# Kernel tuning notes

Measured on AMD Instinct MI355X. Metric: run time of the kernel, lower is better.

## Reference

```python
import jax, jax.numpy as jnp
import numpy as np
from jax import lax

BEAM = 4
MAXLEN = 12
V, E, H = 32000, 256, 512
S, B = 512, 8


def lstm_cell(x, h, c, Wih, Whh, bih, bhh):
    # torch gate order: input, forget, cell, output
    g = x @ Wih.T + h @ Whh.T + bih + bhh
    i, f, gg, o = jnp.split(g, 4, axis=-1)
    c2 = jax.nn.sigmoid(f) * c + jax.nn.sigmoid(i) * jnp.tanh(gg)
    return jax.nn.sigmoid(o) * jnp.tanh(c2), c2


def lstm_layer(xs, Wih, Whh, bih, bhh):
    Bn, Hn = xs.shape[1], Whh.shape[1]
    h0 = jnp.zeros((Bn, Hn), xs.dtype)

    def step(carry, x):
        h, c = carry
        h, c = lstm_cell(x, h, c, Wih, Whh, bih, bhh)
        return (h, c), h

    (hT, cT), hs = lax.scan(step, (h0, h0), xs)
    return hs, hT, cT


def setup_inputs():
    key = jax.random.key(0)
    ks = jax.random.split(key, 32)

    def p(i, shape, s=0.08):
        return jax.random.normal(ks[i], shape, jnp.float32) * s

    return {
        'text': jax.random.randint(ks[0], (S, B), 0, V),
        'emb_enc': p(1, (V, E)),
        'emb_dec': p(2, (V, E)),
        'enc_Wih0': p(3, (4 * H, E)), 'enc_Whh0': p(4, (4 * H, H)),
        'enc_bih0': p(5, (4 * H,)), 'enc_bhh0': p(6, (4 * H,)),
        'enc_Wih1': p(7, (4 * H, H)), 'enc_Whh1': p(8, (4 * H, H)),
        'enc_bih1': p(9, (4 * H,)), 'enc_bhh1': p(10, (4 * H,)),
        'dec_Wih': p(11, (4 * H, E)), 'dec_Whh': p(12, (4 * H, H)),
        'dec_bih': p(13, (4 * H,)), 'dec_bhh': p(14, (4 * H,)),
        'Wq': p(15, (H, H)), 'bq': p(16, (H,)),
        'Wk': p(17, (H, H)), 'bk': p(18, (H,)),
        'Wv': p(19, (H, H)), 'bv': p(20, (H,)),
        'Wo': p(21, (H, H)), 'bo': p(22, (H,)),
        'Wout': p(23, (V, H)), 'bout': p(24, (V,)),
    }


def reference(text, emb_enc, emb_dec, enc_Wih0, enc_Whh0, enc_bih0, enc_bhh0,
              enc_Wih1, enc_Whh1, enc_bih1, enc_bhh1,
              dec_Wih, dec_Whh, dec_bih, dec_bhh,
              Wq, bq, Wk, bk, Wv, bv, Wo, bo, Wout, bout):
    # ---- encoder: 2-layer LSTM over source ----
    emb = emb_enc[text]                                   # [S, B, E]
    hs0, h0, c0 = lstm_layer(emb, enc_Wih0, enc_Whh0, enc_bih0, enc_bhh0)
    hs1, h1, c1 = lstm_layer(hs0, enc_Wih1, enc_Whh1, enc_bih1, enc_bhh1)
    enc_hidden = jnp.stack([h0, h1])                      # [L, B, H] final hidden per layer
    k_enc = enc_hidden @ Wk.T + bk                        # precompute encoder K/V projections
    v_enc = enc_hidden @ Wv.T + bv
    scale = 1.0 / jnp.sqrt(jnp.float32(H))

    # ---- beam state: all beams start from last encoder layer state ----
    dec_h = jnp.tile(h1[None], (BEAM, 1, 1))              # [BEAM, B, H]
    dec_c = jnp.tile(c1[None], (BEAM, 1, 1))
    T = MAXLEN + 1
    result = jnp.full((BEAM, T, B), 1, dtype=jnp.int32)   # SOS token = 1
    logits_hist = jnp.zeros((BEAM, T, B, V), jnp.float32).at[:, 0, :, 1].set(1.0)

    def step(carry, t):
        dh, dc, res, lh = carry
        tok = lax.dynamic_slice(res, (0, t, 0), (BEAM, 1, B))[:, 0, :]      # last token [BEAM, B]
        x = emb_dec[tok]                                                    # [BEAM, B, E]
        nh, nc = lstm_cell(x, dh, dc, dec_Wih, dec_Whh, dec_bih, dec_bhh)   # batched over beams
        # single-head attention: query = dec hidden, keys/values = [enc layers ; dec hidden]
        q = nh @ Wq.T + bq
        kd = nh @ Wk.T + bk
        vd = nh @ Wv.T + bv
        keys = jnp.concatenate([jnp.broadcast_to(k_enc[None], (BEAM,) + k_enc.shape), kd[:, None]], axis=1)  # [BEAM, L+1, B, H]
        vals = jnp.concatenate([jnp.broadcast_to(v_enc[None], (BEAM,) + v_enc.shape), vd[:, None]], axis=1)
        scores = jnp.einsum('nbh,nlbh->nbl', q, keys) * scale
        w = jax.nn.softmax(scores, axis=-1)
        ctx = jnp.einsum('nbl,nlbh->nbh', w, vals)
        dec_out = (ctx @ Wo.T + bo) @ Wout.T + bout                          # [BEAM, B, V]
        # per-beam top-k over vocab, then top-k over the BEAM*BEAM candidates
        pv, pt = lax.top_k(dec_out, BEAM)                                    # [BEAM, B, K]
        cand_v = jnp.transpose(pv, (1, 0, 2)).reshape(B, BEAM * BEAM)        # beam-major blocks
        cand_t = jnp.transpose(pt, (1, 0, 2)).reshape(B, BEAM * BEAM)
        _, ti = lax.top_k(cand_v, BEAM)                                      # [B, K]
        old_beam = (ti // BEAM).T                                            # [BEAM, B]
        new_tok = jnp.take_along_axis(cand_t, ti, axis=1).T                  # [BEAM, B]
        # vectorized beam reorder (gather) of state + history
        nh = jnp.take_along_axis(nh, old_beam[:, :, None], axis=0)
        nc = jnp.take_along_axis(nc, old_beam[:, :, None], axis=0)
        res = jnp.take_along_axis(res, old_beam[:, None, :], axis=0)
        lh = jnp.take_along_axis(lh, old_beam[:, None, :, None], axis=0)
        step_log = jnp.take_along_axis(dec_out, old_beam[:, :, None], axis=0)
        res = lax.dynamic_update_slice(res, new_tok[:, None, :].astype(jnp.int32), (0, t + 1, 0))
        lh = lax.dynamic_update_slice(lh, step_log[:, None], (0, t + 1, 0, 0))
        return (nh, nc, res, lh), None

    (dec_h, dec_c, result, logits_hist), _ = lax.scan(
        step, (dec_h, dec_c, result, logits_hist), jnp.arange(MAXLEN))
    output_res = result[0].T                               # [B, T]
    output_logits = jnp.transpose(logits_hist[0], (1, 2, 0))  # [B, V, T]
    return output_res, output_logits
```

## Files before the change

### kernel.cpp

```cpp
#include <hip/hip_runtime.h>
#include <hip/hip_bf16.h>
#include <float.h>


using ull = unsigned long long;

#define SCOPE_AGENT __HIP_MEMORY_SCOPE_AGENT

__device__ __forceinline__ float cLoad(const float* p) {
  return __hip_atomic_load(p, __ATOMIC_RELAXED, SCOPE_AGENT);
}
__device__ __forceinline__ void cStore(float* p, float v) {
  __hip_atomic_store(p, v, __ATOMIC_RELAXED, SCOPE_AGENT);
}
__device__ __forceinline__ int cLoadI(const int* p) {
  return __hip_atomic_load(p, __ATOMIC_RELAXED, SCOPE_AGENT);
}
__device__ __forceinline__ void cStoreI(int* p, int v) {
  __hip_atomic_store(p, v, __ATOMIC_RELAXED, SCOPE_AGENT);
}
__device__ __forceinline__ ull cLoad64(const ull* p) {
  return __hip_atomic_load(p, __ATOMIC_RELAXED, SCOPE_AGENT);
}
__device__ __forceinline__ void cStore64(ull* p, ull v) {
  __hip_atomic_store(p, v, __ATOMIC_RELAXED, SCOPE_AGENT);
}

__device__ __forceinline__ float2 u2f2(ull u) {
  union { ull u; float2 f; } c; c.u = u; return c.f;
}

__device__ __forceinline__ void fbar1(int* fl, int phase) {
  __syncthreads();
  if (threadIdx.x < 32)
    cStoreI(fl + (blockIdx.x * 32 + threadIdx.x) * 32, phase);
  {
    const int* f = fl + (threadIdx.x * 32 + (blockIdx.x >> 3)) * 32;
    while (cLoadI(f) < phase) {}
  }
  __syncthreads();
}

__device__ __forceinline__ float sig_(float x) { return 1.0f / (1.0f + expf(-x)); }

__device__ __forceinline__ void ins4(float* v, int* id, float nv, int ni) {
  if (nv > v[3] || (nv == v[3] && ni < id[3])) {
    v[3] = nv; id[3] = ni;
#pragma unroll
    for (int p = 3; p > 0; --p) {
      bool sw = (v[p] > v[p - 1]) || (v[p] == v[p - 1] && id[p] < id[p - 1]);
      if (sw) {
        float t0 = v[p]; v[p] = v[p - 1]; v[p - 1] = t0;
        int t1 = id[p]; id[p] = id[p - 1]; id[p - 1] = t1;
      }
    }
  }
}

struct EncP {
  const int* text; const float* emb;
  const float* Wih0; const float* Whh0; const float* bih0; const float* bhh0;
  const float* Wih1; const float* Whh1; const float* bih1; const float* bhh1;
  float* h0buf; float* h1buf; int* regF;
  float* h0f; float* h1f; float* c1f;
};

template <int KX>
__device__ void enc_run(const EncP& P, float* xcat, int w, int tid) {
  constexpr int KTOT = KX + 512;
  constexpr int ST = KTOT + 4;
  constexpr int KSL = KTOT / 8;
  constexpr int Q = KSL / 4;
  constexpr int L = (KX == 512) ? 1 : 0;
  __shared__ float part[16 * 8 * 8];
  __shared__ float gl[128];

  const int c0 = (w & 127) * 4;
  const int kh = tid >> 5, col = (tid >> 3) & 3, b = tid & 7;
  const int kbase = kh * KSL;
  const int rep = w >> 3;

  const float* Wih = L ? P.Wih1 : P.Wih0;
  const float* Whh = L ? P.Whh1 : P.Whh0;
  const float4* wih4[4]; const float4* whh4[4];
#pragma unroll
  for (int g = 0; g < 4; ++g) {
    const int row = g * 512 + c0 + col;
    wih4[g] = (const float4*)(Wih + (size_t)row * KX);
    whh4[g] = (const float4*)(Whh + (size_t)row * 512);
  }
  float bsum = 0.f;
  if (tid < 128) {
    const int r = tid >> 3;
    const int row = (r & 3) * 512 + c0 + (r >> 2);
    bsum = (L ? P.bih1[row] + P.bhh1[row] : P.bih0[row] + P.bhh0[row]);
  }
  float creg = 0.f;
  float* myH = L ? P.h1buf : P.h0buf;

  int qx = (KX - kbase) / 4;
  qx = qx < 0 ? 0 : (qx > Q ? Q : qx);

  for (int e = tid; e < 4096; e += 256)
    xcat[(e >> 9) * ST + KX + (e & 511)] = 0.f;
  __syncthreads();

  for (int i = 0; i <= 512; ++i) {
    const bool act = L ? (i >= 1) : (i < 512);
    if (act) {
      const int t = L ? (i - 1) : i;
      float a0 = 0.f, a1 = 0.f, a2 = 0.f, a3 = 0.f;

      if constexpr (KX == 256) {
        for (int e = tid; e < 1024; e += 256) {
          const int b2 = e >> 7, k2 = e & 127;
          const int tokv = P.text[t * 8 + b2];
          *(float2*)(xcat + b2 * ST + 2 * k2) =
              *(const float2*)(P.emb + (size_t)tokv * 256 + 2 * k2);
        }
        __syncthreads();
        const float4* xq = (const float4*)(xcat + b * ST + kbase);
        const int iw = kbase >> 2;
#pragma unroll 4
        for (int q = 0; q < qx; ++q) {
          float4 x = xq[q];
          float4 w0 = wih4[0][iw + q], w1 = wih4[1][iw + q];
          float4 w2 = wih4[2][iw + q], w3 = wih4[3][iw + q];
          a0 = fmaf(w0.x, x.x, a0); a0 = fmaf(w0.y, x.y, a0);
          a0 = fmaf(w0.z, x.z, a0); a0 = fmaf(w0.w, x.w, a0);
          a1 = fmaf(w1.x, x.x, a1); a1 = fmaf(w1.y, x.y, a1);
          a1 = fmaf(w1.z, x.z, a1); a1 = fmaf(w1.w, x.w, a1);
          a2 = fmaf(w2.x, x.x, a2); a2 = fmaf(w2.y, x.y, a2);
          a2 = fmaf(w2.z, x.z, a2); a2 = fmaf(w2.w, x.w, a2);
          a3 = fmaf(w3.x, x.x, a3); a3 = fmaf(w3.y, x.y, a3);
          a3 = fmaf(w3.z, x.z, a3); a3 = fmaf(w3.w, x.w, a3);
        }
      }

      if (i >= 1) {
        const int s = tid;
        if ((s < 128) || (i >= 2)) {
          const int* f = P.regF + (s * 32 + rep) * 32;
          while (cLoadI(f) < i) __builtin_amdgcn_s_sleep(2);
        }
      }
      __syncthreads();

      if constexpr (KX == 512) {
        const ull* x0 = (const ull*)(P.h0buf + ((i + 1) & 1) * 4096);
        for (int e = tid; e < 2048; e += 256) {
          const int b2 = e >> 8, k2 = e & 255;
          *(ull*)(xcat + b2 * ST + 2 * k2) = cLoad64(x0 + b2 * 256 + k2);
        }
        if (i >= 2) {
          const ull* hq = (const ull*)(P.h1buf + (i & 1) * 4096);
          for (int e = tid; e < 2048; e += 256) {
            const int b2 = e >> 8, k2 = e & 255;
            *(ull*)(xcat + b2 * ST + KX + 2 * k2) = cLoad64(hq + b2 * 256 + k2);
          }
        }
      } else {
        if (i >= 1) {
          const ull* hq = (const ull*)(P.h0buf + ((i + 1) & 1) * 4096);
          for (int e = tid; e < 2048; e += 256) {
            const int b2 = e >> 8, k2 = e & 255;
            *(ull*)(xcat + b2 * ST + KX + 2 * k2) = cLoad64(hq + b2 * 256 + k2);
          }
        }
      }
      __syncthreads();

      {
        const float4* xq = (const float4*)(xcat + b * ST + kbase);
        const int iw = kbase >> 2, ih = (kbase - KX) >> 2;
        if constexpr (KX == 512) {
#pragma unroll 4
          for (int q = 0; q < qx; ++q) {
            float4 x = xq[q];
            float4 w0 = wih4[0][iw + q], w1 = wih4[1][iw + q];
            float4 w2 = wih4[2][iw + q], w3 = wih4[3][iw + q];
            a0 = fmaf(w0.x, x.x, a0); a0 = fmaf(w0.y, x.y, a0);
            a0 = fmaf(w0.z, x.z, a0); a0 = fmaf(w0.w, x.w, a0);
            a1 = fmaf(w1.x, x.x, a1); a1 = fmaf(w1.y, x.y, a1);
            a1 = fmaf(w1.z, x.z, a1); a1 = fmaf(w1.w, x.w, a1);
            a2 = fmaf(w2.x, x.x, a2); a2 = fmaf(w2.y, x.y, a2);
            a2 = fmaf(w2.z, x.z, a2); a2 = fmaf(w2.w, x.w, a2);
            a3 = fmaf(w3.x, x.x, a3); a3 = fmaf(w3.y, x.y, a3);
            a3 = fmaf(w3.z, x.z, a3); a3 = fmaf(w3.w, x.w, a3);
          }
        }
#pragma unroll 4
        for (int q = qx; q < Q; ++q) {
          float4 x = xq[q];
          float4 w0 = whh4[0][ih + q], w1 = whh4[1][ih + q];
          float4 w2 = whh4[2][ih + q], w3 = whh4[3][ih + q];
          a0 = fmaf(w0.x, x.x, a0); a0 = fmaf(w0.y, x.y, a0);
          a0 = fmaf(w0.z, x.z, a0); a0 = fmaf(w0.w, x.w, a0);
          a1 = fmaf(w1.x, x.x, a1); a1 = fmaf(w1.y, x.y, a1);
          a1 = fmaf(w1.z, x.z, a1); a1 = fmaf(w1.w, x.w, a1);
          a2 = fmaf(w2.x, x.x, a2); a2 = fmaf(w2.y, x.y, a2);
          a2 = fmaf(w2.z, x.z, a2); a2 = fmaf(w2.w, x.w, a2);
          a3 = fmaf(w3.x, x.x, a3); a3 = fmaf(w3.y, x.y, a3);
          a3 = fmaf(w3.z, x.z, a3); a3 = fmaf(w3.w, x.w, a3);
        }
      }
      part[((col * 4 + 0) * 8 + b) * 8 + kh] = a0;
      part[((col * 4 + 1) * 8 + b) * 8 + kh] = a1;
      part[((col * 4 + 2) * 8 + b) * 8 + kh] = a2;
      part[((col * 4 + 3) * 8 + b) * 8 + kh] = a3;
      __syncthreads();
      if (tid < 128) {
        const int r = tid >> 3, b2 = tid & 7;
        const float4* pp = (const float4*)(part + (r * 8 + b2) * 8);
        float4 p0 = pp[0], p1 = pp[1];
        gl[r * 8 + b2] =
            bsum + (((p0.x + p0.y) + (p0.z + p0.w)) + ((p1.x + p1.y) + (p1.z + p1.w)));
      }
      __syncthreads();
      if (tid < 32) {
        const int cc = tid >> 3, b2 = tid & 7;
        float gi = gl[(cc * 4 + 0) * 8 + b2], gf_ = gl[(cc * 4 + 1) * 8 + b2];
        float gg = gl[(cc * 4 + 2) * 8 + b2], go = gl[(cc * 4 + 3) * 8 + b2];
        float c2 = sig_(gf_) * creg + sig_(gi) * tanhf(gg);
        float hv = sig_(go) * tanhf(c2);
        creg = c2;
        cStore(myH + (t & 1) * 4096 + b2 * 512 + c0 + cc, hv);
        if (t == 511) {
          (L ? P.h1f : P.h0f)[b2 * 512 + c0 + cc] = hv;
          if (L) P.c1f[b2 * 512 + c0 + cc] = c2;
        }
      }
      __syncthreads();
      if (tid < 32) cStoreI(P.regF + (w * 32 + tid) * 32, i + 1);
    }
  }
}

__global__ __launch_bounds__(256, 1) void enc_kernel(EncP P) {
  __shared__ float xcat0[8 * 772];
  __shared__ float xcat1[8 * 1028];
  if (blockIdx.x >> 7) enc_run<512>(P, xcat1, blockIdx.x, threadIdx.x);
  else enc_run<256>(P, xcat0, blockIdx.x, threadIdx.x);
}

__global__ __launch_bounds__(256) void prep_kernel(
    const float* Wk, const float* bk, const float* Wv, const float* bv,
    const float* h0f, const float* h1f, const float* c1f,
    float* kenc, float* venc, float* nhb, float* ncb) {
  const int w = blockIdx.x, tid = threadIdx.x;
  if (w < 64) {
    const int o = w * 256 + tid;
    const int kv = o >> 13, l = (o >> 12) & 1, b = (o >> 9) & 7, c = o & 511;
    const float4* h4 = (const float4*)((l ? h1f : h0f) + b * 512);
    const float4* w4 = (const float4*)((kv ? Wv : Wk) + (size_t)c * 512);
    float s0 = 0.f, s1 = 0.f, s2 = 0.f, s3 = 0.f;
#pragma unroll 8
    for (int k = 0; k < 128; ++k) {
      float4 a = w4[k], x = h4[k];
      s0 = fmaf(a.x, x.x, s0); s1 = fmaf(a.y, x.y, s1);
      s2 = fmaf(a.z, x.z, s2); s3 = fmaf(a.w, x.w, s3);
    }
    (kv ? venc : kenc)[l * 4096 + b * 512 + c] =
        (kv ? bv : bk)[c] + ((s0 + s1) + (s2 + s3));
  } else {
    const int o = (w - 64) * 256 + tid;
    nhb[16384 + o] = h1f[o & 4095];
    ncb[16384 + o] = c1f[o & 4095];
  }
}

__global__ __launch_bounds__(256) void prep2_kernel(
    const float* Wq, const float* Wk, const float* Wv, const float* Wo,
    const float* bq, const float* bk, const float* bv,
    const float* kenc, const float* venc,
    float* At, float* W2, float* u, float* pvec, float* veWo, float* bvo,
    float* sl0, float* sbb) {
  const int w = blockIdx.x, tid = threadIdx.x;
#pragma unroll 1
  for (int sub = 0; sub < 2; ++sub) {
    const int d = 2 * w + sub;
    for (int cc = 0; cc < 2; ++cc) {
      const int c = tid + cc * 256;
      float s0 = 0.f, s1 = 0.f, s2 = 0.f, s3 = 0.f;
      for (int i = 0; i < 512; i += 4) {
        s0 = fmaf(Wk[(i + 0) * 512 + d], Wq[(i + 0) * 512 + c], s0);
        s1 = fmaf(Wk[(i + 1) * 512 + d], Wq[(i + 1) * 512 + c], s1);
        s2 = fmaf(Wk[(i + 2) * 512 + d], Wq[(i + 2) * 512 + c], s2);
        s3 = fmaf(Wk[(i + 3) * 512 + d], Wq[(i + 3) * 512 + c], s3);
      }
      At[(size_t)d * 512 + c] = (s0 + s1) + (s2 + s3);
    }
    for (int cc = 0; cc < 2; ++cc) {
      const int dc = tid + cc * 256;
      float s0 = 0.f, s1 = 0.f, s2 = 0.f, s3 = 0.f;
      const float* wor = Wo + (size_t)d * 512;
      for (int c2 = 0; c2 < 512; c2 += 4) {
        s0 = fmaf(wor[c2 + 0], Wv[(size_t)(c2 + 0) * 512 + dc], s0);
        s1 = fmaf(wor[c2 + 1], Wv[(size_t)(c2 + 1) * 512 + dc], s1);
        s2 = fmaf(wor[c2 + 2], Wv[(size_t)(c2 + 2) * 512 + dc], s2);
        s3 = fmaf(wor[c2 + 3], Wv[(size_t)(c2 + 3) * 512 + dc], s3);
      }
      W2[(size_t)d * 512 + dc] = (s0 + s1) + (s2 + s3);
    }
  }
  if (w == 0) {
    for (int cc = 0; cc < 2; ++cc) {
      const int c = tid + cc * 256;
      float a = 0.f;
      for (int i = 0; i < 512; ++i)
        a += Wq[i * 512 + c] * bk[i] + Wk[i * 512 + c] * bq[i];
      u[c] = a;
    }
  } else if (w <= 32) {
    const int idx = (w - 1) * 256 + tid;
    const int l = idx >> 12, b = (idx >> 9) & 7, c = idx & 511;
    const float* ke = kenc + l * 4096 + b * 512;
    float a = 0.f;
    for (int i = 0; i < 512; ++i) a = fmaf(Wq[i * 512 + c], ke[i], a);
    pvec[idx] = a;
  } else if (w <= 64) {
    const int idx = (w - 33) * 256 + tid;
    const int l = idx >> 12, b = (idx >> 9) & 7, j = idx & 511;
    const float* ve = venc + l * 4096 + b * 512;
    const float* wo = Wo + (size_t)j * 512;
    float a = 0.f;
    for (int c = 0; c < 512; ++c) a = fmaf(wo[c], ve[c], a);
    veWo[idx] = a;
  } else if (w == 65) {
    for (int cc = 0; cc < 2; ++cc) {
      const int j = tid + cc * 256;
      const float* wo = Wo + (size_t)j * 512;
      float a = 0.f;
      for (int c = 0; c < 512; ++c) a = fmaf(wo[c], bv[c], a);
      bvo[j] = a;
    }
  } else if (w == 66) {
    if (tid < 16) {
      const int l = tid >> 3, b = tid & 7;
      const float* ke = kenc + l * 4096 + b * 512;
      float a = 0.f;
      for (int i = 0; i < 512; ++i) a = fmaf(bq[i], ke[i], a);
      sl0[tid] = a;
    } else if (tid == 16) {
      float a = 0.f;
      for (int i = 0; i < 512; ++i) a = fmaf(bq[i], bk[i], a);
      sbb[0] = a;
    }
  }
}

__global__ __launch_bounds__(256) void prep3_kernel(
    const float* Wout, const float* bout, const float* bo, const float* veWo,
    float* E0g, float* E1g, float* bcg) {
  __shared__ float sv[16 * 516 + 512];
  __shared__ float stg[8 * 516];
  const int w = blockIdx.x, tid = threadIdx.x;
  for (int e = tid; e < 8704; e += 256) {
    if (e < 8192) sv[(e >> 9) * 516 + (e & 511)] = veWo[e];
    else sv[16 * 516 + (e - 8192)] = bo[e - 8192];
  }
  const int cbase = w * 125;
  for (int tile = 0; tile < 16; ++tile) {
    const int r0 = tile * 8;
    __syncthreads();
    for (int e = tid; e < 1024; e += 256) {
      const int rr = e >> 7, k4 = e & 127;
      int row = r0 + rr; if (row > 124) row = 124;
      *(float4*)&stg[rr * 516 + k4 * 4] =
          *(const float4*)&Wout[(size_t)(cbase + row) * 512 + k4 * 4];
    }
    __syncthreads();
    if (tid < 136) {
      const int rr = tid / 17, sel = tid - rr * 17;
      const int row = r0 + rr;
      if (row < 125) {
        const float4* a4 = (const float4*)&stg[rr * 516];
        const float4* x4 =
            (const float4*)&sv[sel < 16 ? sel * 516 : 16 * 516];
        float s0 = 0.f, s1 = 0.f, s2 = 0.f, s3 = 0.f;
#pragma unroll 8
        for (int k = 0; k < 128; ++k) {
          float4 a = a4[k], x = x4[k];
          s0 = fmaf(a.x, x.x, s0); s1 = fmaf(a.y, x.y, s1);
          s2 = fmaf(a.z, x.z, s2); s3 = fmaf(a.w, x.w, s3);
        }
        const float s = (s0 + s1) + (s2 + s3);
        const int c = cbase + row;
        if (sel < 16) (sel < 8 ? E0g : E1g)[(size_t)(sel & 7) * 32000 + c] = s;
        else bcg[c] = s + bout[c];
      }
    }
  }
}

struct DecP {
  const float* emb;
  const float* Wih; const float* Whh; const float* bih; const float* bhh;
  const float* Wout;
  const float* At; const float* W2; const float* u; const float* bvo;
  const float* pvec; const float* sl0; const float* sbb;
  const float* E0g; const float* E1g; const float* bcg;
  float* nhb; float* ncb;
  float* vbuf;
  float* part_s;
  ull* pvp;
  int* obh;
  int* res0;
  __hip_bfloat16* hist;
  int* fl;
};

__global__ __launch_bounds__(256, 1) void dec_kernel(DecP P) {
  __shared__ float SM[29600];
  __shared__ float gl[2][4][32];
  __shared__ float slS[32][3];
  __shared__ float wslS[96];
  __shared__ float svv[32][8][4];
  __shared__ int sii[32][8][4];
  __shared__ float rvS[32][4];
  __shared__ int rtS[32][4];
  __shared__ int resS[4][13][8];
  __shared__ int oblS[32];
  __shared__ int tokS[32];
  __shared__ float pscS[32][8];
  __shared__ float nhsS[32][8];

  const int w = blockIdx.x, tid = threadIdx.x;
  float* hs = SM;
  float* tileS = SM;
  float* vqS = SM + 16896;
  float* tvE = SM + 21120;
  int* tiE = (int*)(SM + 25344);
  int ph = 0;

  if (tid < 104) {
    for (int n = 0; n < 4; ++n) resS[n][tid >> 3][tid & 7] = 1;
  }

  auto do_select = [&](int tt) {
    {
      const int r = tid >> 3, ch = tid & 7;
      float m4[4] = {-FLT_MAX, -FLT_MAX, -FLT_MAX, -FLT_MAX};
      int mi[4] = {0x7fffffff, 0x7fffffff, 0x7fffffff, 0x7fffffff};
      for (int g = 0; g < 4; ++g) {
        ull pk[32];
#pragma unroll
        for (int z = 0; z < 32; ++z) {
          const int wg = ch * 32 + g * 8 + (z >> 2);
          pk[z] = cLoad64(P.pvp + wg * 128 + r * 4 + (z & 3));
        }
#pragma unroll
        for (int z = 0; z < 32; ++z)
          ins4(m4, mi, __uint_as_float((unsigned)(pk[z] >> 32)),
               (int)(unsigned)(pk[z] & 0xffffffffu));
      }
#pragma unroll
      for (int k = 0; k < 4; ++k) { svv[r][ch][k] = m4[k]; sii[r][ch][k] = mi[k]; }
    }
    __syncthreads();
    if (tid < 32) {
      float m4[4] = {-FLT_MAX, -FLT_MAX, -FLT_MAX, -FLT_MAX};
      int mi[4] = {0x7fffffff, 0x7fffffff, 0x7fffffff, 0x7fffffff};
      for (int g2 = 0; g2 < 8; ++g2)
#pragma unroll
        for (int k = 0; k < 4; ++k) ins4(m4, mi, svv[tid][g2][k], sii[tid][g2][k]);
#pragma unroll
      for (int k = 0; k < 4; ++k) { rvS[tid][k] = m4[k]; rtS[tid][k] = mi[k]; }
    }
    __syncthreads();
    if (tid < 8) {
      const int b2 = tid;
      unsigned used = 0;
      int obl_[4], tkl_[4];
#pragma unroll
      for (int sel = 0; sel < 4; ++sel) {
        float bestv = -FLT_MAX; int bestj = -1;
        for (int j = 0; j < 16; ++j) {
          if (used & (1u << j)) continue;
          float vv = rvS[(j >> 2) * 8 + b2][j & 3];
          if (vv > bestv) { bestv = vv; bestj = j; }
        }
        used |= 1u << bestj;
        const int obn = bestj >> 2;
        obl_[sel] = obn;
        tkl_[sel] = rtS[obn * 8 + b2][bestj & 3];
        oblS[sel * 8 + b2] = obn;
        tokS[sel * 8 + b2] = tkl_[sel];
        if (w == 0) P.obh[tt * 32 + sel * 8 + b2] = obn;
      }
      if (w == 0) {
        int tmp[4][13];
        for (int n2 = 0; n2 < 4; ++n2)
          for (int s2 = 0; s2 < 13; ++s2) tmp[n2][s2] = resS[obl_[n2]][s2][b2];
        for (int n2 = 0; n2 < 4; ++n2)
          for (int s2 = 0; s2 < 13; ++s2) resS[n2][s2][b2] = tmp[n2][s2];
        for (int n2 = 0; n2 < 4; ++n2) resS[n2][tt + 1][b2] = tkl_[n2];
      }
    }
    __syncthreads();
    if (tt == 11 && w == 0 && tid < 104)
      P.res0[tid] = resS[0][tid >> 3][tid & 7];
  };

  for (int t = 0; t < 12; ++t) {
    const int curOff = (t & 1) * 16384, prevOff = ((t + 1) & 1) * 16384;

    if (t == 0) {
      __syncthreads();
      if (tid < 32) { oblS[tid] = tid >> 3; tokS[tid] = 1; }
      __syncthreads();
    } else {
      do_select(t - 1);
    }
    {
      const int col_l = tid >> 7, gate = (tid >> 5) & 3, nb = tid & 31;
      const int col = 2 * w + col_l;
      const int row = gate * 512 + col;
      for (int e = tid; e < 2048; e += 256) {
        const int nb2 = e >> 6, kf = e & 63;
        float4 v = *((const float4*)(P.emb + (size_t)tokS[nb2] * 256) + kf);
        *((float4*)hs + nb2 * 65 + kf) = v;
      }
      __syncthreads();
      float s0 = 0.f, s1 = 0.f, s2 = 0.f, s3 = 0.f;
      {
        const float4* a4 = (const float4*)(P.Wih + (size_t)row * 256);
        const float4* x4 = (const float4*)hs + nb * 65;
#pragma unroll 8
        for (int k = 0; k < 64; ++k) {
          float4 a = a4[k], x = x4[k];
          s0 = fmaf(a.x, x.x, s0); s1 = fmaf(a.y, x.y, s1);
          s2 = fmaf(a.z, x.z, s2); s3 = fmaf(a.w, x.w, s3);
        }
      }
      float acc = P.bih[row] + P.bhh[row];
      const ull* hsrc = (const ull*)(P.nhb + prevOff);
      const float4* w4row = (const float4*)(P.Whh + (size_t)row * 512);
      for (int ck = 0; ck < 2; ++ck) {
        __syncthreads();
        for (int e = tid; e < 4096; e += 256) {
          const int nb2 = e >> 7, k2 = e & 127;
          const int srow = oblS[nb2] * 8 + (nb2 & 7);
          ull v = cLoad64(hsrc + srow * 256 + ck * 128 + k2);
          *(ull*)(hs + nb2 * 260 + 2 * k2) = v;
        }
        __syncthreads();
        const float4* h4 = (const float4*)hs + nb * 65;
        const float4* w4 = w4row + ck * 64;
#pragma unroll 8
        for (int k = 0; k < 64; ++k) {
          float4 a = w4[k], x = h4[k];
          s0 = fmaf(a.x, x.x, s0); s1 = fmaf(a.y, x.y, s1);
          s2 = fmaf(a.z, x.z, s2); s3 = fmaf(a.w, x.w, s3);
        }
      }
      acc += (s0 + s1) + (s2 + s3);
      gl[col_l][gate][nb] = acc;
      __syncthreads();
      if (tid < 64) {
        const int cc = tid >> 5, nb2 = tid & 31;
        const int col2 = 2 * w + cc;
        float gi = gl[cc][0][nb2], gf_ = gl[cc][1][nb2];
        float gg = gl[cc][2][nb2], go = gl[cc][3][nb2];
        const int srow = oblS[nb2] * 8 + (nb2 & 7);
        float cold = cLoad(P.ncb + prevOff + srow * 512 + col2);
        float c2 = sig_(gf_) * cold + sig_(gi) * tanhf(gg);
        float hv = sig_(go) * tanhf(c2);
        cStore(P.nhb + curOff + nb2 * 512 + col2, hv);
        cStore(P.ncb + curOff + nb2 * 512 + col2, c2);
      }
    }
    fbar1(P.fl, ++ph);

    if (w < 128) {
      const int p = w >> 6, cb = w & 63;
      const int col_l = tid >> 5, nb = tid & 31;
      const int col = cb * 8 + col_l;
      const float* W = (p ? P.W2 : P.At) + (size_t)col * 512;
      float acc = (p ? P.bvo : P.u)[col];
      {
        const float4* w4row = (const float4*)W;
        float s0 = 0.f, s1 = 0.f, s2 = 0.f, s3 = 0.f;
        for (int ck = 0; ck < 2; ++ck) {
          __syncthreads();
          const ull* s8 = (const ull*)(P.nhb + curOff);
          for (int e = tid; e < 4096; e += 256) {
            const int nb2 = e >> 7, k2 = e & 127;
            ull v = cLoad64(s8 + nb2 * 256 + ck * 128 + k2);
            *(ull*)(hs + nb2 * 260 + 2 * k2) = v;
          }
          __syncthreads();
          const float4* h4 = (const float4*)hs + nb * 65;
          const float4* w4 = w4row + ck * 64;
#pragma unroll 8
          for (int k = 0; k < 64; ++k) {
            float4 a = w4[k], x = h4[k];
            s0 = fmaf(a.x, x.x, s0); s1 = fmaf(a.y, x.y, s1);
            s2 = fmaf(a.z, x.z, s2); s3 = fmaf(a.w, x.w, s3);
          }
        }
        acc += (s0 + s1) + (s2 + s3);
      }
      if (p) {
        cStore(P.vbuf + nb * 512 + col, acc);
      } else {
        const float nhv = cLoad(P.nhb + curOff + nb * 512 + col);
        pscS[nb][col_l] = nhv * acc;
        nhsS[nb][col_l] = nhv;
        __syncthreads();
        if (tid < 32) {
          const int nb2 = tid, b = nb2 & 7;
          float s2a = 0.f, l0 = 0.f, l1 = 0.f;
#pragma unroll
          for (int i2 = 0; i2 < 8; ++i2) {
            s2a += pscS[nb2][i2];
            const float nv = nhsS[nb2][i2];
            l0 = fmaf(nv, P.pvec[b * 512 + cb * 8 + i2], l0);
            l1 = fmaf(nv, P.pvec[4096 + b * 512 + cb * 8 + i2], l1);
          }
          cStore(P.part_s + (0 * 32 + nb2) * 64 + cb, l0);
          cStore(P.part_s + (1 * 32 + nb2) * 64 + cb, l1);
          cStore(P.part_s + (2 * 32 + nb2) * 64 + cb, s2a);
        }
      }
    }
    fbar1(P.fl, ++ph);

    {
      const int cbase = w * 125;
      if (tid < 96) {
        const int nb = tid / 3, l = tid - (tid / 3) * 3, b = nb & 7;
        const ull* ps = (const ull*)(P.part_s + (l * 32 + nb) * 64);
        ull pk[32];
#pragma unroll
        for (int z = 0; z < 32; ++z) pk[z] = cLoad64(ps + z);
        float s = 0.f;
#pragma unroll
        for (int z = 0; z < 32; ++z) { float2 f = u2f2(pk[z]); s += f.x + f.y; }
        const float bias = (l < 2) ? P.sl0[l * 8 + b] : P.sbb[0];
        slS[nb][l] = (s + bias) * (1.0f / sqrtf(512.0f));
      }
      __syncthreads();
      if (tid < 32) {
        float a = slS[tid][0], b2 = slS[tid][1], c3 = slS[tid][2];
        float m = fmaxf(a, fmaxf(b2, c3));
        float e0 = expf(a - m), e1 = expf(b2 - m), e2 = expf(c3 - m);
        float inv = 1.0f / (e0 + e1 + e2);
        wslS[tid * 3 + 0] = e0 * inv;
        wslS[tid * 3 + 1] = e1 * inv;
        wslS[tid * 3 + 2] = e2 * inv;
      }
      const int rg = tid >> 3, ng = tid & 7;
      float acc[4][4];
#pragma unroll
      for (int i = 0; i < 4; ++i)
#pragma unroll
        for (int j = 0; j < 4; ++j) acc[i][j] = 0.f;
      for (int q = 0; q < 4; ++q) {
        __syncthreads();
        for (int e = tid; e < 1024; e += 256) {
          const int nb = e >> 5, kf = e & 31;
          ull u0 = cLoad64((const ull*)(P.vbuf + nb * 512 + q * 128 + kf * 4));
          ull u1 = cLoad64((const ull*)(P.vbuf + nb * 512 + q * 128 + kf * 4 + 2));
          float2 a = u2f2(u0), b2 = u2f2(u1);
          float4 v = {a.x, a.y, b2.x, b2.y};
          *(float4*)(vqS + (nb & 3) * 1056 + (nb >> 2) * 132 + kf * 4) = v;
        }
        for (int it = 0; it < 16; ++it) {
          const int idx = it * 256 + tid;
          if (idx < 4000) {
            const int r = idx >> 5, kf = idx & 31;
            float4 v = *(const float4*)(P.Wout + (size_t)(cbase + r) * 512 +
                                        q * 128 + kf * 4);
            *(float4*)(tileS + (r & 3) * 4224 + (r >> 2) * 132 + kf * 4) = v;
          }
        }
        __syncthreads();
        for (int kf = 0; kf < 32; ++kf) {
          float4 xv[4], wv[4];
#pragma unroll
          for (int j = 0; j < 4; ++j)
            xv[j] = *(const float4*)(vqS + j * 1056 + ng * 132 + kf * 4);
#pragma unroll
          for (int i = 0; i < 4; ++i)
            wv[i] = *(const float4*)(tileS + i * 4224 + rg * 132 + kf * 4);
#pragma unroll
          for (int i = 0; i < 4; ++i)
#pragma unroll
            for (int j = 0; j < 4; ++j) {
              float a = acc[i][j];
              a = fmaf(wv[i].x, xv[j].x, a); a = fmaf(wv[i].y, xv[j].y, a);
              a = fmaf(wv[i].z, xv[j].z, a); a = fmaf(wv[i].w, xv[j].w, a);
              acc[i][j] = a;
            }
        }
      }
      __syncthreads();
      float w0w[4], w1w[4], w2w[4];
#pragma unroll
      for (int j = 0; j < 4; ++j) {
        const int nb = ng * 4 + j;
        w0w[j] = wslS[nb * 3 + 0]; w1w[j] = wslS[nb * 3 + 1]; w2w[j] = wslS[nb * 3 + 2];
      }
      float v4[4][4]; int i4[4][4];
#pragma unroll
      for (int j = 0; j < 4; ++j)
#pragma unroll
        for (int k = 0; k < 4; ++k) { v4[j][k] = -FLT_MAX; i4[j][k] = 0x7fffffff; }
#pragma unroll
      for (int i = 0; i < 4; ++i) {
        const int r = rg * 4 + i;
        if (r < 125) {
          const int c = cbase + r;
          const float bcv = P.bcg[c];
#pragma unroll
          for (int j = 0; j < 4; ++j) {
            const int nb = ng * 4 + j, b = nb & 7;
            const float e0 = P.E0g[(size_t)b * 32000 + c];
            const float e1 = P.E1g[(size_t)b * 32000 + c];
            const float L = fmaf(w2w[j], acc[i][j],
                                 fmaf(w0w[j], e0, fmaf(w1w[j], e1, bcv)));
            P.hist[(size_t)t * 1024000 + (size_t)nb * 32000 + c] = __float2bfloat16(L);
            ins4(v4[j], i4[j], L, c);
          }
        }
      }
#pragma unroll
      for (int j = 0; j < 4; ++j)
#pragma unroll
        for (int k = 0; k < 4; ++k) {
          tvE[(ng * 4 + j) * 132 + rg * 4 + k] = v4[j][k];
          tiE[(ng * 4 + j) * 132 + rg * 4 + k] = i4[j][k];
        }
      __syncthreads();
      if (tid < 32) {
        float m4[4] = {-FLT_MAX, -FLT_MAX, -FLT_MAX, -FLT_MAX};
        int mi[4] = {0x7fffffff, 0x7fffffff, 0x7fffffff, 0x7fffffff};
        for (int e = 0; e < 128; ++e)
          ins4(m4, mi, tvE[tid * 132 + e], tiE[tid * 132 + e]);
#pragma unroll
        for (int k = 0; k < 4; ++k) {
          ull pk = ((ull)__float_as_uint(m4[k]) << 32) | (unsigned)mi[k];
          cStore64(P.pvp + w * 128 + tid * 4 + k, pk);
        }
      }
    }
    fbar1(P.fl, ++ph);
  }
  if (w == 0) do_select(11);
}

__global__ __launch_bounds__(256) void out_kernel(const __hip_bfloat16* hist,
                                                  const int* obh, const int* res0,
                                                  float* out) {
  __shared__ float sh[13 * 1000];
  __shared__ int sbArr[12];
  const int w = blockIdx.x, tid = threadIdx.x;
  const int b = w >> 5, v0 = (w & 31) * 1000;
  if (tid == 0) {
    int beta = 0;
    for (int t = 11; t >= 0; --t) {
      const int sb = obh[t * 32 + beta * 8 + b];
      sbArr[t] = sb;
      beta = sb;
    }
  }
  __syncthreads();
  for (int e = tid; e < 12000; e += 256) {
    const int t = e / 1000, vv = e - t * 1000;
    sh[(t + 1) * 1000 + vv] = __bfloat162float(
        hist[(size_t)(t * 32 + sbArr[t] * 8 + b) * 32000 + v0 + vv]);
  }
  for (int e = tid; e < 1000; e += 256) sh[e] = (v0 + e == 1) ? 1.0f : 0.0f;
  __syncthreads();
  float* base = out + 104 + (size_t)(b * 32000 + v0) * 13;
  for (int o = tid; o < 13000; o += 256) {
    const int v = o / 13, t = o - v * 13;
    base[o] = sh[t * 1000 + v];
  }
  if (w == 0 && tid < 104) {
    out[(tid & 7) * 13 + (tid >> 3)] = (float)res0[tid];
  }
}

extern "C" void kernel_launch(void* const* d_in, const int* in_sizes, int n_in,
                              void* d_out, int out_size, void* d_ws, size_t ws_size,
                              hipStream_t stream) {
  const int* text  = (const int*)d_in[0];
  const float* embE = (const float*)d_in[1];
  const float* embD = (const float*)d_in[2];
  const float* Wih0 = (const float*)d_in[3];
  const float* Whh0 = (const float*)d_in[4];
  const float* bih0 = (const float*)d_in[5];
  const float* bhh0 = (const float*)d_in[6];
  const float* Wih1 = (const float*)d_in[7];
  const float* Whh1 = (const float*)d_in[8];
  const float* bih1 = (const float*)d_in[9];
  const float* bhh1 = (const float*)d_in[10];
  const float* dWih = (const float*)d_in[11];
  const float* dWhh = (const float*)d_in[12];
  const float* dbih = (const float*)d_in[13];
  const float* dbhh = (const float*)d_in[14];
  const float* Wq = (const float*)d_in[15];
  const float* bq = (const float*)d_in[16];
  const float* Wk = (const float*)d_in[17];
  const float* bk = (const float*)d_in[18];
  const float* Wv = (const float*)d_in[19];
  const float* bv = (const float*)d_in[20];
  const float* Wo = (const float*)d_in[21];
  const float* bo = (const float*)d_in[22];
  const float* Wout = (const float*)d_in[23];
  const float* bout = (const float*)d_in[24];

  char* ws = (char*)d_ws;
  size_t off = 0;
  auto alloc = [&](size_t bytes) -> char* {
    off = (off + 511) & ~(size_t)511;
    char* p = ws + off;
    off += bytes;
    return p;
  };
  float* h0buf = (float*)alloc(2 * 4096 * 4);
  float* h1buf = (float*)alloc(2 * 4096 * 4);
  int* regF   = (int*)alloc((size_t)262144 * 4);
  int* decFl  = (int*)alloc((size_t)262144 * 4);
  float* h0f  = (float*)alloc(4096 * 4);
  float* h1f  = (float*)alloc(4096 * 4);
  float* c1f  = (float*)alloc(4096 * 4);
  float* kenc = (float*)alloc(8192 * 4);
  float* venc = (float*)alloc(8192 * 4);
  float* At   = (float*)alloc((size_t)262144 * 4);
  float* W2   = (float*)alloc((size_t)262144 * 4);
  float* u    = (float*)alloc(512 * 4);
  float* pvec = (float*)alloc(8192 * 4);
  float* veWo = (float*)alloc(8192 * 4);
  float* bvo  = (float*)alloc(512 * 4);
  float* sl0  = (float*)alloc(16 * 4);
  float* sbb  = (float*)alloc(32 * 4);
  float* E0g  = (float*)alloc((size_t)256000 * 4);
  float* E1g  = (float*)alloc((size_t)256000 * 4);
  float* bcg  = (float*)alloc(32000 * 4);
  float* nhb  = (float*)alloc(2 * 16384 * 4);
  float* ncb  = (float*)alloc(2 * 16384 * 4);
  float* vbuf = (float*)alloc(16384 * 4);
  float* part_s = (float*)alloc(6144 * 4);
  ull* pvp    = (ull*)alloc((size_t)32768 * 8);
  int* obh    = (int*)alloc(384 * 4);
  int* res0   = (int*)alloc(104 * 4);
  __hip_bfloat16* hist = (__hip_bfloat16*)alloc((size_t)12288000 * 2);
  if (off > ws_size) return;

  hipMemsetAsync(regF, 0, (size_t)262144 * 4, stream);
  hipMemsetAsync(decFl, 0, (size_t)262144 * 4, stream);

  EncP ep{text, embE, Wih0, Whh0, bih0, bhh0, Wih1, Whh1, bih1, bhh1,
          h0buf, h1buf, regF, h0f, h1f, c1f};
  enc_kernel<<<256, 256, 0, stream>>>(ep);

  prep_kernel<<<128, 256, 0, stream>>>(Wk, bk, Wv, bv, h0f, h1f, c1f, kenc, venc,
                                       nhb, ncb);
  prep2_kernel<<<256, 256, 0, stream>>>(Wq, Wk, Wv, Wo, bq, bk, bv, kenc, venc,
                                        At, W2, u, pvec, veWo, bvo, sl0, sbb);
  prep3_kernel<<<256, 256, 0, stream>>>(Wout, bout, bo, veWo, E0g, E1g, bcg);

  DecP dp{embD, dWih, dWhh, dbih, dbhh, Wout,
          At, W2, u, bvo, pvec, sl0, sbb, E0g, E1g, bcg,
          nhb, ncb, vbuf, part_s, pvp, obh, res0, hist, decFl};
  dec_kernel<<<256, 256, 0, stream>>>(dp);

  out_kernel<<<256, 256, 0, stream>>>(hist, obh, res0, (float*)d_out);
}
```

Baseline: 6.959 ms.

## Replace encoder flag barriers with sentinel-polled full hidden-state history

The encoder LSTM stops using per-step flag barriers and double-buffered hidden states. Every timestep's h is now written to a full history buffer pre-filled with a 0xFF NaN sentinel, and consumers poll the data itself until the sentinel is gone. This removes the flag stores, the flag polling and one __syncthreads per step, and lets layer 1 trail layer 0 with some slack. In exchange it adds two memsets of about 8 MB each and reads that spin on data, and it relies on a real hidden value never matching the sentinel pattern.

```diff
diff --git a/kernel.cpp b/kernel.cpp
--- a/kernel.cpp
+++ b/kernel.cpp
@@ -28,6 +28,13 @@
 
 __device__ __forceinline__ float2 u2f2(ull u) {
   union { ull u; float2 f; } c; c.u = u; return c.f;
+}
+
+__device__ __forceinline__ ull pollLoad(const ull* p) {
+  ull v = cLoad64(p);
+  while ((unsigned)v == 0xFFFFFFFFu || (unsigned)(v >> 32) == 0xFFFFFFFFu)
+    v = cLoad64(p);
+  return v;
 }
 
 __device__ __forceinline__ void fbar1(int* fl, int phase) {
@@ -61,7 +68,7 @@
   const int* text; const float* emb;
   const float* Wih0; const float* Whh0; const float* bih0; const float* bhh0;
   const float* Wih1; const float* Whh1; const float* bih1; const float* bhh1;
-  float* h0buf; float* h1buf; int* regF;
+  float* h0hist; float* h1hist;
   float* h0f; float* h1f; float* c1f;
 };
 
@@ -78,7 +85,6 @@
   const int c0 = (w & 127) * 4;
   const int kh = tid >> 5, col = (tid >> 3) & 3, b = tid & 7;
   const int kbase = kh * KSL;
-  const int rep = w >> 3;
 
   const float* Wih = L ? P.Wih1 : P.Wih0;
   const float* Whh = L ? P.Whh1 : P.Whh0;
@@ -96,7 +102,7 @@
     bsum = (L ? P.bih1[row] + P.bhh1[row] : P.bih0[row] + P.bhh0[row]);
   }
   float creg = 0.f;
-  float* myH = L ? P.h1buf : P.h0buf;
+  float* myHist = L ? P.h1hist : P.h0hist;
 
   int qx = (KX - kbase) / 4;
   qx = qx < 0 ? 0 : (qx > Q ? Q : qx);
@@ -105,134 +111,90 @@
     xcat[(e >> 9) * ST + KX + (e & 511)] = 0.f;
   __syncthreads();
 
-  for (int i = 0; i <= 512; ++i) {
-    const bool act = L ? (i >= 1) : (i < 512);
-    if (act) {
-      const int t = L ? (i - 1) : i;
-      float a0 = 0.f, a1 = 0.f, a2 = 0.f, a3 = 0.f;
-
-      if constexpr (KX == 256) {
-        for (int e = tid; e < 1024; e += 256) {
-          const int b2 = e >> 7, k2 = e & 127;
-          const int tokv = P.text[t * 8 + b2];
-          *(float2*)(xcat + b2 * ST + 2 * k2) =
-              *(const float2*)(P.emb + (size_t)tokv * 256 + 2 * k2);
-        }
-        __syncthreads();
-        const float4* xq = (const float4*)(xcat + b * ST + kbase);
-        const int iw = kbase >> 2;
+  for (int t = 0; t < 512; ++t) {
+    if constexpr (KX == 256) {
+      for (int e = tid; e < 1024; e += 256) {
+        const int b2 = e >> 7, k2 = e & 127;
+        const int tokv = P.text[t * 8 + b2];
+        *(float2*)(xcat + b2 * ST + 2 * k2) =
+            *(const float2*)(P.emb + (size_t)tokv * 256 + 2 * k2);
+      }
+    } else {
+      const ull* x0 = (const ull*)(P.h0hist + (size_t)(t + 1) * 4096);
+      for (int e = tid; e < 2048; e += 256) {
+        const int b2 = e >> 8, k2 = e & 255;
+        *(ull*)(xcat + b2 * ST + 2 * k2) = pollLoad(x0 + b2 * 256 + k2);
+      }
+    }
+    if (t >= 1) {
+      const ull* hq = (const ull*)(myHist + (size_t)t * 4096);
+      for (int e = tid; e < 2048; e += 256) {
+        const int b2 = e >> 8, k2 = e & 255;
+        *(ull*)(xcat + b2 * ST + KX + 2 * k2) = pollLoad(hq + b2 * 256 + k2);
+      }
+    }
+    __syncthreads();
+
+    float a0 = 0.f, a1 = 0.f, a2 = 0.f, a3 = 0.f;
+    {
+      const float4* xq = (const float4*)(xcat + b * ST + kbase);
+      const int iw = kbase >> 2, ih = (kbase - KX) >> 2;
 #pragma unroll 4
-        for (int q = 0; q < qx; ++q) {
-          float4 x = xq[q];
-          float4 w0 = wih4[0][iw + q], w1 = wih4[1][iw + q];
-          float4 w2 = wih4[2][iw + q], w3 = wih4[3][iw + q];
-          a0 = fmaf(w0.x, x.x, a0); a0 = fmaf(w0.y, x.y, a0);
-          a0 = fmaf(w0.z, x.z, a0); a0 = fmaf(w0.w, x.w, a0);
-          a1 = fmaf(w1.x, x.x, a1); a1 = fmaf(w1.y, x.y, a1);
-          a1 = fmaf(w1.z, x.z, a1); a1 = fmaf(w1.w, x.w, a1);
-          a2 = fmaf(w2.x, x.x, a2); a2 = fmaf(w2.y, x.y, a2);
-          a2 = fmaf(w2.z, x.z, a2); a2 = fmaf(w2.w, x.w, a2);
-          a3 = fmaf(w3.x, x.x, a3); a3 = fmaf(w3.y, x.y, a3);
-          a3 = fmaf(w3.z, x.z, a3); a3 = fmaf(w3.w, x.w, a3);
-        }
-      }
-
-      if (i >= 1) {
-        const int s = tid;
-        if ((s < 128) || (i >= 2)) {
-          const int* f = P.regF + (s * 32 + rep) * 32;
-          while (cLoadI(f) < i) __builtin_amdgcn_s_sleep(2);
-        }
-      }
-      __syncthreads();
-
-      if constexpr (KX == 512) {
-        const ull* x0 = (const ull*)(P.h0buf + ((i + 1) & 1) * 4096);
-        for (int e = tid; e < 2048; e += 256) {
-          const int b2 = e >> 8, k2 = e & 255;
-          *(ull*)(xcat + b2 * ST + 2 * k2) = cLoad64(x0 + b2 * 256 + k2);
-        }
-        if (i >= 2) {
-          const ull* hq = (const ull*)(P.h1buf + (i & 1) * 4096);
-          for (int e = tid; e < 2048; e += 256) {
-            const int b2 = e >> 8, k2 = e & 255;
-            *(ull*)(xcat + b2 * ST + KX + 2 * k2) = cLoad64(hq + b2 * 256 + k2);
-          }
-        }
-      } else {
-        if (i >= 1) {
-          const ull* hq = (const ull*)(P.h0buf + ((i + 1) & 1) * 4096);
-          for (int e = tid; e < 2048; e += 256) {
-            const int b2 = e >> 8, k2 = e & 255;
-            *(ull*)(xcat + b2 * ST + KX + 2 * k2) = cLoad64(hq + b2 * 256 + k2);
-          }
-        }
-      }
-      __syncthreads();
-
-      {
-        const float4* xq = (const float4*)(xcat + b * ST + kbase);
-        const int iw = kbase >> 2, ih = (kbase - KX) >> 2;
-        if constexpr (KX == 512) {
+      for (int q = 0; q < qx; ++q) {
+        float4 x = xq[q];
+        float4 w0 = wih4[0][iw + q], w1 = wih4[1][iw + q];
+        float4 w2 = wih4[2][iw + q], w3 = wih4[3][iw + q];
+        a0 = fmaf(w0.x, x.x, a0); a0 = fmaf(w0.y, x.y, a0);
+        a0 = fmaf(w0.z, x.z, a0); a0 = fmaf(w0.w, x.w, a0);
+        a1 = fmaf(w1.x, x.x, a1); a1 = fmaf(w1.y, x.y, a1);
+        a1 = fmaf(w1.z, x.z, a1); a1 = fmaf(w1.w, x.w, a1);
+        a2 = fmaf(w2.x, x.x, a2); a2 = fmaf(w2.y, x.y, a2);
+        a2 = fmaf(w2.z, x.z, a2); a2 = fmaf(w2.w, x.w, a2);
+        a3 = fmaf(w3.x, x.x, a3); a3 = fmaf(w3.y, x.y, a3);
+        a3 = fmaf(w3.z, x.z, a3); a3 = fmaf(w3.w, x.w, a3);
+      }
 #pragma unroll 4
-          for (int q = 0; q < qx; ++q) {
-            float4 x = xq[q];
-            float4 w0 = wih4[0][iw + q], w1 = wih4[1][iw + q];
-            float4 w2 = wih4[2][iw + q], w3 = wih4[3][iw + q];
-            a0 = fmaf(w0.x, x.x, a0); a0 = fmaf(w0.y, x.y, a0);
-            a0 = fmaf(w0.z, x.z, a0); a0 = fmaf(w0.w, x.w, a0);
-            a1 = fmaf(w1.x, x.x, a1); a1 = fmaf(w1.y, x.y, a1);
-            a1 = fmaf(w1.z, x.z, a1); a1 = fmaf(w1.w, x.w, a1);
-            a2 = fmaf(w2.x, x.x, a2); a2 = fmaf(w2.y, x.y, a2);
-            a2 = fmaf(w2.z, x.z, a2); a2 = fmaf(w2.w, x.w, a2);
-            a3 = fmaf(w3.x, x.x, a3); a3 = fmaf(w3.y, x.y, a3);
-            a3 = fmaf(w3.z, x.z, a3); a3 = fmaf(w3.w, x.w, a3);
-          }
-        }
-#pragma unroll 4
-        for (int q = qx; q < Q; ++q) {
-          float4 x = xq[q];
-          float4 w0 = whh4[0][ih + q], w1 = whh4[1][ih + q];
-          float4 w2 = whh4[2][ih + q], w3 = whh4[3][ih + q];
-          a0 = fmaf(w0.x, x.x, a0); a0 = fmaf(w0.y, x.y, a0);
-          a0 = fmaf(w0.z, x.z, a0); a0 = fmaf(w0.w, x.w, a0);
-          a1 = fmaf(w1.x, x.x, a1); a1 = fmaf(w1.y, x.y, a1);
-          a1 = fmaf(w1.z, x.z, a1); a1 = fmaf(w1.w, x.w, a1);
-          a2 = fmaf(w2.x, x.x, a2); a2 = fmaf(w2.y, x.y, a2);
-          a2 = fmaf(w2.z, x.z, a2); a2 = fmaf(w2.w, x.w, a2);
-          a3 = fmaf(w3.x, x.x, a3); a3 = fmaf(w3.y, x.y, a3);
-          a3 = fmaf(w3.z, x.z, a3); a3 = fmaf(w3.w, x.w, a3);
-        }
-      }
-      part[((col * 4 + 0) * 8 + b) * 8 + kh] = a0;
-      part[((col * 4 + 1) * 8 + b) * 8 + kh] = a1;
-      part[((col * 4 + 2) * 8 + b) * 8 + kh] = a2;
-      part[((col * 4 + 3) * 8 + b) * 8 + kh] = a3;
-      __syncthreads();
-      if (tid < 128) {
-        const int r = tid >> 3, b2 = tid & 7;
-        const float4* pp = (const float4*)(part + (r * 8 + b2) * 8);
-        float4 p0 = pp[0], p1 = pp[1];
-        gl[r * 8 + b2] =
-            bsum + (((p0.x + p0.y) + (p0.z + p0.w)) + ((p1.x + p1.y) + (p1.z + p1.w)));
-      }
-      __syncthreads();
-      if (tid < 32) {
-        const int cc = tid >> 3, b2 = tid & 7;
-        float gi = gl[(cc * 4 + 0) * 8 + b2], gf_ = gl[(cc * 4 + 1) * 8 + b2];
-        float gg = gl[(cc * 4 + 2) * 8 + b2], go = gl[(cc * 4 + 3) * 8 + b2];
-        float c2 = sig_(gf_) * creg + sig_(gi) * tanhf(gg);
-        float hv = sig_(go) * tanhf(c2);
-        creg = c2;
-        cStore(myH + (t & 1) * 4096 + b2 * 512 + c0 + cc, hv);
-        if (t == 511) {
-          (L ? P.h1f : P.h0f)[b2 * 512 + c0 + cc] = hv;
-          if (L) P.c1f[b2 * 512 + c0 + cc] = c2;
-        }
-      }
-      __syncthreads();
-      if (tid < 32) cStoreI(P.regF + (w * 32 + tid) * 32, i + 1);
-    }
+      for (int q = qx; q < Q; ++q) {
+        float4 x = xq[q];
+        float4 w0 = whh4[0][ih + q], w1 = whh4[1][ih + q];
+        float4 w2 = whh4[2][ih + q], w3 = whh4[3][ih + q];
+        a0 = fmaf(w0.x, x.x, a0); a0 = fmaf(w0.y, x.y, a0);
+        a0 = fmaf(w0.z, x.z, a0); a0 = fmaf(w0.w, x.w, a0);
+        a1 = fmaf(w1.x, x.x, a1); a1 = fmaf(w1.y, x.y, a1);
+        a1 = fmaf(w1.z, x.z, a1); a1 = fmaf(w1.w, x.w, a1);
+        a2 = fmaf(w2.x, x.x, a2); a2 = fmaf(w2.y, x.y, a2);
+        a2 = fmaf(w2.z, x.z, a2); a2 = fmaf(w2.w, x.w, a2);
+        a3 = fmaf(w3.x, x.x, a3); a3 = fmaf(w3.y, x.y, a3);
+        a3 = fmaf(w3.z, x.z, a3); a3 = fmaf(w3.w, x.w, a3);
+      }
+    }
+    part[((col * 4 + 0) * 8 + b) * 8 + kh] = a0;
+    part[((col * 4 + 1) * 8 + b) * 8 + kh] = a1;
+    part[((col * 4 + 2) * 8 + b) * 8 + kh] = a2;
+    part[((col * 4 + 3) * 8 + b) * 8 + kh] = a3;
+    __syncthreads();
+    if (tid < 128) {
+      const int r = tid >> 3, b2 = tid & 7;
+      const float4* pp = (const float4*)(part + (r * 8 + b2) * 8);
+      float4 p0 = pp[0], p1 = pp[1];
+      gl[r * 8 + b2] =
+          bsum + (((p0.x + p0.y) + (p0.z + p0.w)) + ((p1.x + p1.y) + (p1.z + p1.w)));
+    }
+    __syncthreads();
+    if (tid < 32) {
+      const int cc = tid >> 3, b2 = tid & 7;
+      float gi = gl[(cc * 4 + 0) * 8 + b2], gf_ = gl[(cc * 4 + 1) * 8 + b2];
+      float gg = gl[(cc * 4 + 2) * 8 + b2], go = gl[(cc * 4 + 3) * 8 + b2];
+      float c2 = sig_(gf_) * creg + sig_(gi) * tanhf(gg);
+      float hv = sig_(go) * tanhf(c2);
+      creg = c2;
+      cStore(myHist + (size_t)(t + 1) * 4096 + b2 * 512 + c0 + cc, hv);
+      if (t == 511) {
+        (L ? P.h1f : P.h0f)[b2 * 512 + c0 + cc] = hv;
+        if (L) P.c1f[b2 * 512 + c0 + cc] = c2;
+      }
+    }
+    __syncthreads();
   }
 }
 
@@ -820,9 +782,8 @@
     off += bytes;
     return p;
   };
-  float* h0buf = (float*)alloc(2 * 4096 * 4);
-  float* h1buf = (float*)alloc(2 * 4096 * 4);
-  int* regF   = (int*)alloc((size_t)262144 * 4);
+  float* h0hist = (float*)alloc((size_t)513 * 4096 * 4);
+  float* h1hist = (float*)alloc((size_t)513 * 4096 * 4);
   int* decFl  = (int*)alloc((size_t)262144 * 4);
   float* h0f  = (float*)alloc(4096 * 4);
   float* h1f  = (float*)alloc(4096 * 4);
@@ -850,11 +811,12 @@
   __hip_bfloat16* hist = (__hip_bfloat16*)alloc((size_t)12288000 * 2);
   if (off > ws_size) return;
 
-  hipMemsetAsync(regF, 0, (size_t)262144 * 4, stream);
+  hipMemsetAsync(h0hist, 0xFF, (size_t)513 * 4096 * 4, stream);
+  hipMemsetAsync(h1hist, 0xFF, (size_t)513 * 4096 * 4, stream);
   hipMemsetAsync(decFl, 0, (size_t)262144 * 4, stream);
 
   EncP ep{text, embE, Wih0, Whh0, bih0, bhh0, Wih1, Whh1, bih1, bhh1,
-          h0buf, h1buf, regF, h0f, h1f, c1f};
+          h0hist, h1hist, h0f, h1f, c1f};
   enc_kernel<<<256, 256, 0, stream>>>(ep);
 
   prep_kernel<<<128, 256, 0, stream>>>(Wk, bk, Wv, bv, h0f, h1f, c1f, kenc, venc,
```

Result: faster. 6.623 ms (-4.8%).
